# Kernel tuning notes

Measured on AMD Instinct MI355X. Metric: run time of the kernel, lower is better.

The kernel has to match this reference:

```python
import jax, jax.numpy as jnp
import numpy as np

B, N, M = 2, 2048, 1024
C, CTX, H = 1024, 1024, 16
D = C // H
HID = int(C * 4.0)
EPS = 1e-6


def _ln(h):
    # LayerNorm32: fp32 layernorm, eps=1e-6, no affine params
    h32 = h.astype(jnp.float32)
    mu = jnp.mean(h32, axis=-1, keepdims=True)
    var = jnp.var(h32, axis=-1, keepdims=True)
    return ((h32 - mu) * jax.lax.rsqrt(var + EPS)).astype(h.dtype)


def _sdpa(q, k, v):
    # q: [B,Q,H,D], k/v: [B,K,H,D]
    scale = 1.0 / np.sqrt(D)
    s = jnp.einsum('bqhd,bkhd->bhqk', q, k) * scale
    p = jax.nn.softmax(s, axis=-1)
    return jnp.einsum('bhqk,bkhd->bqhd', p, v)


def _forward(x, context, Wqkv, bqkv, Wos, bos, Wq, bq, Wkv, bkv, Woc, boc, W1, b1, W2, b2):
    Bx, Nx, _ = x.shape
    Mx = context.shape[1]
    # --- self-attention (attn_mode='full') ---
    h = _ln(x)
    qkv = (h @ Wqkv + bqkv).reshape(Bx, Nx, 3, H, D)
    q, k, v = qkv[:, :, 0], qkv[:, :, 1], qkv[:, :, 2]
    a = _sdpa(q, k, v).reshape(Bx, Nx, C)
    x = x + (a @ Wos + bos)
    # --- cross-attention (always 'full') ---
    h = _ln(x)
    q = (h @ Wq + bq).reshape(Bx, Nx, H, D)
    kv = (context @ Wkv + bkv).reshape(Bx, Mx, 2, H, D)
    k, v = kv[:, :, 0], kv[:, :, 1]
    a = _sdpa(q, k, v).reshape(Bx, Nx, C)
    x = x + (a @ Woc + boc)
    # --- FFN with tanh-approx GELU ---
    h = _ln(x)
    x = x + (jax.nn.gelu(h @ W1 + b1, approximate=True) @ W2 + b2)
    return x


def setup_inputs() -> dict:
    key = jax.random.key(0)
    ks = jax.random.split(key, 12)
    rn = lambda k, shape: (jax.random.normal(k, shape, jnp.float32) * 0.02)
    return {
        'x': jax.random.normal(ks[0], (B, N, C), jnp.float32),
        'context': jax.random.normal(ks[1], (B, M, CTX), jnp.float32),
        'Wqkv': rn(ks[2], (C, 3 * C)), 'bqkv': jnp.zeros((3 * C,), jnp.float32),
        'Wos': rn(ks[3], (C, C)), 'bos': jnp.zeros((C,), jnp.float32),
        'Wq': rn(ks[4], (C, C)), 'bq': jnp.zeros((C,), jnp.float32),
        'Wkv': rn(ks[5], (CTX, 2 * C)), 'bkv': jnp.zeros((2 * C,), jnp.float32),
        'Woc': rn(ks[6], (C, C)), 'boc': jnp.zeros((C,), jnp.float32),
        'W1': rn(ks[7], (C, HID)), 'b1': jnp.zeros((HID,), jnp.float32),
        'W2': rn(ks[8], (HID, C)), 'b2': jnp.zeros((C,), jnp.float32),
    }


def reference(x, context, Wqkv, bqkv, Wos, bos, Wq, bq, Wkv, bkv, Woc, boc, W1, b1, W2, b2):
    return _forward(x, context, Wqkv, bqkv, Wos, bos, Wq, bq, Wkv, bkv, Woc, boc, W1, b1, W2, b2)
```

## Files before the change

### kernel.cpp

```cpp
#include <hip/hip_runtime.h>
#include <cstdint>

typedef unsigned short u16;
typedef short bf16x8 __attribute__((ext_vector_type(8)));
typedef unsigned short u16x8 __attribute__((ext_vector_type(8)));
typedef float f32x4 __attribute__((ext_vector_type(4)));

__device__ __forceinline__ u16 f2bf(float f) {
  union { float f; uint32_t u; } v; v.f = f;
  uint32_t r = (v.u + 0x7fffu + ((v.u >> 16) & 1u)) >> 16;
  return (u16)r;
}

__device__ __forceinline__ void gload_lds16(const u16* g, u16* l) {
  __builtin_amdgcn_global_load_lds(
      (const __attribute__((address_space(1))) void*)g,
      (__attribute__((address_space(3))) void*)l, 16, 0, 0);
}

__global__ __launch_bounds__(256) void ln_kernel(const float* __restrict__ x,
                                                 u16* __restrict__ h) {
  const int row = blockIdx.x;
  const int tid = threadIdx.x;
  const float4 v = *reinterpret_cast<const float4*>(x + (long)row * 1024 + tid * 4);
  float s  = v.x + v.y + v.z + v.w;
  float ss = v.x * v.x + v.y * v.y + v.z * v.z + v.w * v.w;
#pragma unroll
  for (int off = 32; off >= 1; off >>= 1) {
    s  += __shfl_xor(s, off, 64);
    ss += __shfl_xor(ss, off, 64);
  }
  __shared__ float red[8];
  const int wave = tid >> 6, lane = tid & 63;
  if (lane == 0) { red[wave] = s; red[4 + wave] = ss; }
  __syncthreads();
  s  = red[0] + red[1] + red[2] + red[3];
  ss = red[4] + red[5] + red[6] + red[7];
  const float mu   = s * (1.0f / 1024.0f);
  const float var  = ss * (1.0f / 1024.0f) - mu * mu;
  const float rstd = rsqrtf(var + 1e-6f);
  ushort4 o;
  o.x = f2bf((v.x - mu) * rstd);
  o.y = f2bf((v.y - mu) * rstd);
  o.z = f2bf((v.z - mu) * rstd);
  o.w = f2bf((v.w - mu) * rstd);
  *reinterpret_cast<ushort4*>(h + (long)row * 1024 + tid * 4) = o;
}

struct WEnt { const float* W; u16* Wt; int K, N, tEnd; };
struct WEnts { WEnt e[7]; int n; };

__global__ __launch_bounds__(256) void wconvert_all(WEnts args) {
  __shared__ u16 tile[64][72];
  int t = blockIdx.x;
  int i = 0, tStart = 0;
  while (i < args.n - 1 && t >= args.e[i].tEnd) { tStart = args.e[i].tEnd; i++; }
  const float* W = args.e[i].W;
  u16* Wt = args.e[i].Wt;
  const int K = args.e[i].K, N = args.e[i].N;
  const int rel = t - tStart;
  const int ntn = N >> 6;
  const int tn = rel % ntn, tk = rel / ntn;
  const int n0 = tn * 64, k0 = tk * 64;

  const int th = threadIdx.x;
  const int c4 = (th & 15) * 4;
  const int r  = th >> 4;
#pragma unroll
  for (int ii = 0; ii < 4; ii++) {
    const int row = ii * 16 + r;
    const float4 v = *reinterpret_cast<const float4*>(W + (long)(k0 + row) * N + n0 + c4);
    tile[c4 + 0][row] = f2bf(v.x);
    tile[c4 + 1][row] = f2bf(v.y);
    tile[c4 + 2][row] = f2bf(v.z);
    tile[c4 + 3][row] = f2bf(v.w);
  }
  __syncthreads();
  const int c8 = (th & 7) * 8;
  const int rn = th >> 3;
#pragma unroll
  for (int ii = 0; ii < 2; ii++) {
    const int row = ii * 32 + rn;
    *reinterpret_cast<u16x8*>(Wt + (long)(n0 + row) * K + k0 + c8) =
        *reinterpret_cast<const u16x8*>(&tile[row][c8]);
  }
}

__global__ __launch_bounds__(256) void f2bf_kernel(const float* __restrict__ in,
                                                   u16* __restrict__ out) {
  const long i = ((long)blockIdx.x * 256 + threadIdx.x) * 4;
  const float4 v = *reinterpret_cast<const float4*>(in + i);
  ushort4 o;
  o.x = f2bf(v.x); o.y = f2bf(v.y); o.z = f2bf(v.z); o.w = f2bf(v.w);
  *reinterpret_cast<ushort4*>(out + i) = o;
}

__global__ __launch_bounds__(256) void vtrans(const u16* __restrict__ V,
                                              u16* __restrict__ Vt,
                                              int vStride, long vBatch, int nk) {
  __shared__ u16 tile[64][72];
  const int t = threadIdx.x;
  const int b = blockIdx.z, h = blockIdx.y, n0 = blockIdx.x * 64;
  const u16* vp = V + (long)b * vBatch + h * 64;
  u16* op = Vt + (long)(b * 16 + h) * 64 * (long)nk + n0;
  const int ch = t & 7;
#pragma unroll
  for (int i = 0; i < 2; i++) {
    const int n = (t >> 3) + i * 32;
    const u16x8 v = *reinterpret_cast<const u16x8*>(vp + (long)(n0 + n) * vStride + ch * 8);
#pragma unroll
    for (int j = 0; j < 8; j++) tile[ch * 8 + j][n] = v[j];
  }
  __syncthreads();
#pragma unroll
  for (int i = 0; i < 2; i++) {
    const int d = (t >> 3) + i * 32;
    *reinterpret_cast<u16x8*>(op + (long)d * nk + ch * 8) =
        *reinterpret_cast<const u16x8*>(&tile[d][ch * 8]);
  }
}

template <int TN, int SX, bool OUT_BF16, bool GELU_ACT, bool RES>
__global__ __launch_bounds__(256, 2) void gemm_bt(
    const u16* __restrict__ A, const u16* __restrict__ Bt,
    const float* __restrict__ bias, const float* __restrict__ res,
    void* __restrict__ Cout, int Ndim, int Kdim, int lx, int ly) {
  constexpr int NFRAG = TN / 32;
  __shared__ u16 Al[2][128 * 32];
  __shared__ u16 Bl[2][TN * 32];
  const int j = blockIdx.x;
  const int c = j & 7, kk = j >> 3;
  const int cx = c % SX, cy = c / SX;
  const int bx = cx * lx + (kk % lx);
  const int by = cy * ly + (kk / lx);
  const int m0 = by * 128, n0 = bx * TN;

  const int tid  = threadIdx.x;
  const int lane = tid & 63, wave = tid >> 6;
  const int quad = lane >> 4, l15 = lane & 15;
  const int wr = wave >> 1, wc = wave & 1;

  f32x4 acc[4][NFRAG];
  const f32x4 vzero = {0.f, 0.f, 0.f, 0.f};
#pragma unroll
  for (int i = 0; i < 4; i++)
#pragma unroll
    for (int jj = 0; jj < NFRAG; jj++) acc[i][jj] = vzero;

  const long rowOff = (long)(lane >> 2) * Kdim + (lane & 3) * 8;
  const u16* gA = A  + (long)m0 * Kdim + rowOff;
  const u16* gB = Bt + (long)n0 * Kdim + rowOff;

  auto stage = [&](int k0, int p) {
    gload_lds16(gA + (long)(wave * 16) * Kdim + k0,       &Al[p][wave * 512]);
    gload_lds16(gA + (long)((wave + 4) * 16) * Kdim + k0, &Al[p][(wave + 4) * 512]);
    gload_lds16(gB + (long)(wave * 16) * Kdim + k0,       &Bl[p][wave * 512]);
    if constexpr (TN == 128)
      gload_lds16(gB + (long)((wave + 4) * 16) * Kdim + k0, &Bl[p][(wave + 4) * 512]);
  };

  stage(0, 0);
  int p = 0;
  for (int k0 = 0; k0 < Kdim; k0 += 32, p ^= 1) {
    __syncthreads();
    bf16x8 af[4], bfr[NFRAG];
#pragma unroll
    for (int mt = 0; mt < 4; mt++)
      af[mt] = *reinterpret_cast<const bf16x8*>(&Al[p][(wr * 64 + mt * 16 + l15) * 32 + quad * 8]);
#pragma unroll
    for (int nt = 0; nt < NFRAG; nt++)
      bfr[nt] = *reinterpret_cast<const bf16x8*>(&Bl[p][(wc * NFRAG * 16 + nt * 16 + l15) * 32 + quad * 8]);
    if (k0 + 32 < Kdim) stage(k0 + 32, p ^ 1);
#pragma unroll
    for (int mt = 0; mt < 4; mt++)
#pragma unroll
      for (int nt = 0; nt < NFRAG; nt++)
        acc[mt][nt] = __builtin_amdgcn_mfma_f32_16x16x32_bf16(af[mt], bfr[nt], acc[mt][nt], 0, 0, 0);
  }

#pragma unroll
  for (int nt = 0; nt < NFRAG; nt++) {
    const int col = n0 + wc * NFRAG * 16 + nt * 16 + l15;
    const float bv = bias[col];
#pragma unroll
    for (int mt = 0; mt < 4; mt++) {
#pragma unroll
      for (int r = 0; r < 4; r++) {
        const int row = m0 + wr * 64 + mt * 16 + quad * 4 + r;
        float y = acc[mt][nt][r] + bv;
        if (GELU_ACT) {
          const float t = 0.7978845608028654f * (y + 0.044715f * y * y * y);
          y = 0.5f * y * (1.0f + tanhf(t));
        }
        if (RES) y += res[(long)row * Ndim + col];
        if (OUT_BF16)
          ((u16*)Cout)[(long)row * Ndim + col] = f2bf(y);
        else
          ((float*)Cout)[(long)row * Ndim + col] = y;
      }
    }
  }
}

__global__ __launch_bounds__(256, 2) void attn_kernel(
    const u16* __restrict__ Q, const u16* __restrict__ K, const u16* __restrict__ Vt,
    u16* __restrict__ O, int nk, int qStride, int kStride, int oStride,
    long qBatch, long kBatch, long oBatch) {
  __shared__ u16 Kt[2][64 * 64];
  __shared__ u16 Vl[2][64 * 64];
  __shared__ u16 Pl[4][32 * 64];

  const int tid = threadIdx.x;
  const int lane = tid & 63, wave = tid >> 6;
  const int quad = lane >> 4, l15 = lane & 15;
  const int b = blockIdx.z, hh = blockIdx.y, qt = blockIdx.x;

  const u16* qp = Q + (long)b * qBatch + hh * 64;
  const u16* kp = K + (long)b * kBatch + hh * 64;
  const u16* vp = Vt + (long)(b * 16 + hh) * 64 * (long)nk;

  bf16x8 qf[2][2];
  const int qrow = qt * 128 + wave * 32 + l15;
#pragma unroll
  for (int qg = 0; qg < 2; qg++) {
    qf[qg][0] = *reinterpret_cast<const bf16x8*>(qp + (long)(qrow + qg * 16) * qStride + quad * 8);
    qf[qg][1] = *reinterpret_cast<const bf16x8*>(qp + (long)(qrow + qg * 16) * qStride + 32 + quad * 8);
  }

  const int r8 = lane >> 3;
  const int gcol = ((lane & 7) ^ r8) * 8;
  const u16* kgA = kp + (long)(wave * 8 + r8) * kStride + gcol;
  const u16* kgB = kp + (long)((wave + 4) * 8 + r8) * kStride + gcol;
  const u16* vgA = vp + (long)(wave * 8 + r8) * nk + gcol;
  const u16* vgB = vp + (long)((wave + 4) * 8 + r8) * nk + gcol;

  const int cF = (quad ^ (l15 & 7)) * 8;

  const f32x4 vzero = {0.f, 0.f, 0.f, 0.f};
  f32x4 oAcc[2][4];
  float lSt[2] = {0.f, 0.f};
#pragma unroll
  for (int qg = 0; qg < 2; qg++)
#pragma unroll
    for (int i = 0; i < 4; i++) oAcc[qg][i] = vzero;

  const float SCL = 0.18033688f;
  const int nTiles = nk >> 6;
  const long kAdv = (long)64 * kStride;

  auto stage = [&](int kt, int p) {
    gload_lds16(kgA + kt * kAdv, &Kt[p][wave * 512]);
    gload_lds16(kgB + kt * kAdv, &Kt[p][(wave + 4) * 512]);
    gload_lds16(vgA + kt * 64,   &Vl[p][wave * 512]);
    gload_lds16(vgB + kt * 64,   &Vl[p][(wave + 4) * 512]);
  };

  stage(0, 0);
  int p = 0;
  for (int kt = 0; kt < nTiles; kt++, p ^= 1) {
    __syncthreads();
    if (kt + 1 < nTiles) stage(kt + 1, p ^ 1);

    f32x4 st[2][4];
#pragma unroll
    for (int mt = 0; mt < 4; mt++) {
      const bf16x8 kf0 = *reinterpret_cast<const bf16x8*>(&Kt[p][(mt * 16 + l15) * 64 + cF]);
      const bf16x8 kf1 = *reinterpret_cast<const bf16x8*>(&Kt[p][(mt * 16 + l15) * 64 + (cF ^ 32)]);
#pragma unroll
      for (int qg = 0; qg < 2; qg++) {
        f32x4 z = vzero;
        z = __builtin_amdgcn_mfma_f32_16x16x32_bf16(kf0, qf[qg][0], z, 0, 0, 0);
        z = __builtin_amdgcn_mfma_f32_16x16x32_bf16(kf1, qf[qg][1], z, 0, 0, 0);
        st[qg][mt] = z;
      }
    }

#pragma unroll
    for (int qg = 0; qg < 2; qg++) {
      float ps = 0.f;
#pragma unroll
      for (int mt = 0; mt < 4; mt++)
#pragma unroll
        for (int r = 0; r < 4; r++) {
          const float pw = __builtin_amdgcn_exp2f(st[qg][mt][r] * SCL);
          st[qg][mt][r] = pw;
          ps += pw;
        }
      lSt[qg] += ps;
      u16* plw = &Pl[wave][(qg * 16 + l15) * 64];
#pragma unroll
      for (int mt = 0; mt < 4; mt++) {
        union { float f; uint32_t u; } a0, a1, a2, a3;
        a0.f = st[qg][mt][0]; a1.f = st[qg][mt][1];
        a2.f = st[qg][mt][2]; a3.f = st[qg][mt][3];
        a0.u += 0x8000u; a1.u += 0x8000u; a2.u += 0x8000u; a3.u += 0x8000u;
        uint2 w;
        w.x = __builtin_amdgcn_perm(a1.u, a0.u, 0x07060302u);
        w.y = __builtin_amdgcn_perm(a3.u, a2.u, 0x07060302u);
        const int pcol = (((mt * 2 + (quad >> 1)) ^ (l15 & 7)) * 8) + (quad & 1) * 4;
        *reinterpret_cast<uint2*>(&plw[pcol]) = w;
      }
    }

    bf16x8 pf[2][2];
#pragma unroll
    for (int qg = 0; qg < 2; qg++) {
      const u16* plw = &Pl[wave][(qg * 16 + l15) * 64];
      pf[qg][0] = *reinterpret_cast<const bf16x8*>(&plw[cF]);
      pf[qg][1] = *reinterpret_cast<const bf16x8*>(&plw[cF ^ 32]);
    }
#pragma unroll
    for (int dt = 0; dt < 4; dt++) {
      const bf16x8 vf0 = *reinterpret_cast<const bf16x8*>(&Vl[p][(dt * 16 + l15) * 64 + cF]);
      const bf16x8 vf1 = *reinterpret_cast<const bf16x8*>(&Vl[p][(dt * 16 + l15) * 64 + (cF ^ 32)]);
#pragma unroll
      for (int qg = 0; qg < 2; qg++) {
        oAcc[qg][dt] = __builtin_amdgcn_mfma_f32_16x16x32_bf16(pf[qg][0], vf0, oAcc[qg][dt], 0, 0, 0);
        oAcc[qg][dt] = __builtin_amdgcn_mfma_f32_16x16x32_bf16(pf[qg][1], vf1, oAcc[qg][dt], 0, 0, 0);
      }
    }
  }

  u16* op = O + (long)b * oBatch + hh * 64;
#pragma unroll
  for (int qg = 0; qg < 2; qg++) {
    float l = lSt[qg];
    l += __shfl_xor(l, 16, 64);
    l += __shfl_xor(l, 32, 64);
    float lR[4];
#pragma unroll
    for (int r = 0; r < 4; r++) lR[r] = 1.0f / __shfl(l, quad * 4 + r, 64);
#pragma unroll
    for (int dt = 0; dt < 4; dt++)
#pragma unroll
      for (int r = 0; r < 4; r++) {
        const int row = qt * 128 + wave * 32 + qg * 16 + quad * 4 + r;
        op[(long)row * oStride + dt * 16 + l15] = f2bf(oAcc[qg][dt][r] * lR[r]);
      }
  }
}

extern "C" void kernel_launch(void* const* d_in, const int* in_sizes, int n_in,
                              void* d_out, int out_size, void* d_ws, size_t ws_size,
                              hipStream_t stream) {
  const float* x    = (const float*)d_in[0];
  const float* ctx  = (const float*)d_in[1];
  const float* Wqkv = (const float*)d_in[2];
  const float* bqkv = (const float*)d_in[3];
  const float* Wos  = (const float*)d_in[4];
  const float* bos  = (const float*)d_in[5];
  const float* Wq   = (const float*)d_in[6];
  const float* bq   = (const float*)d_in[7];
  const float* Wkv  = (const float*)d_in[8];
  const float* bkv  = (const float*)d_in[9];
  const float* Woc  = (const float*)d_in[10];
  const float* boc  = (const float*)d_in[11];
  const float* W1   = (const float*)d_in[12];
  const float* b1   = (const float*)d_in[13];
  const float* W2   = (const float*)d_in[14];
  const float* b2   = (const float*)d_in[15];
  float* out = (float*)d_out;
  char* ws = (char*)d_ws;
  const size_t MB = 1024 * 1024;

  if (ws_size >= 80 * MB) {
    u16* Wqkvt = (u16*)(ws + 0 * MB);
    u16* Wost  = (u16*)(ws + 6 * MB);
    u16* Wqt   = (u16*)(ws + 8 * MB);
    u16* Wkvt  = (u16*)(ws + 10 * MB);
    u16* Woct  = (u16*)(ws + 14 * MB);
    u16* W1t   = (u16*)(ws + 16 * MB);
    u16* W2t   = (u16*)(ws + 24 * MB);
    u16* h     = (u16*)(ws + 32 * MB);
    u16* abuf  = (u16*)(ws + 40 * MB);
    u16* qkv   = (u16*)(ws + 48 * MB);
    u16* q2    = (u16*)(ws + 48 * MB);
    u16* kv2   = (u16*)(ws + 56 * MB);
    u16* ctxbf = (u16*)(ws + 64 * MB);
    u16* VtCr  = (u16*)(ws + 68 * MB);
    u16* hid   = (u16*)(ws + 48 * MB);
    u16* VtSelf = h;

    WEnts we;
    we.n = 7;
    we.e[0] = {Wqkv, Wqkvt, 1024, 3072, 768};
    we.e[1] = {Wos,  Wost,  1024, 1024, 1024};
    we.e[2] = {Wq,   Wqt,   1024, 1024, 1280};
    we.e[3] = {Wkv,  Wkvt,  1024, 2048, 1792};
    we.e[4] = {Woc,  Woct,  1024, 1024, 2048};
    we.e[5] = {W1,   W1t,   1024, 4096, 3072};
    we.e[6] = {W2,   W2t,   4096, 1024, 4096};
    wconvert_all<<<dim3(4096), dim3(256), 0, stream>>>(we);
    f2bf_kernel<<<dim3(2048), dim3(256), 0, stream>>>(ctx, ctxbf);

    ln_kernel<<<dim3(4096), dim3(256), 0, stream>>>(x, h);
    gemm_bt<128, 2, true, false, false><<<dim3(768), dim3(256), 0, stream>>>(
        h, Wqkvt, bqkv, nullptr, qkv, 3072, 1024, 12, 8);
    vtrans<<<dim3(32, 16, 2), dim3(256), 0, stream>>>(
        qkv + 2048, VtSelf, 3072, (long)2048 * 3072, 2048);
    attn_kernel<<<dim3(16, 16, 2), dim3(256), 0, stream>>>(
        qkv, qkv + 1024, VtSelf, abuf, 2048, 3072, 3072, 1024,
        (long)2048 * 3072, (long)2048 * 3072, (long)2048 * 1024);
    gemm_bt<64, 1, false, false, true><<<dim3(512), dim3(256), 0, stream>>>(
        abuf, Wost, bos, x, out, 1024, 1024, 16, 4);
    ln_kernel<<<dim3(4096), dim3(256), 0, stream>>>(out, h);
    gemm_bt<64, 1, true, false, false><<<dim3(512), dim3(256), 0, stream>>>(
        h, Wqt, bq, nullptr, q2, 1024, 1024, 16, 4);
    gemm_bt<64, 2, true, false, false><<<dim3(512), dim3(256), 0, stream>>>(
        ctxbf, Wkvt, bkv, nullptr, kv2, 2048, 1024, 16, 4);
    vtrans<<<dim3(16, 16, 2), dim3(256), 0, stream>>>(
        kv2 + 1024, VtCr, 2048, (long)1024 * 2048, 1024);
    attn_kernel<<<dim3(16, 16, 2), dim3(256), 0, stream>>>(
        q2, kv2, VtCr, abuf, 1024, 1024, 2048, 1024,
        (long)2048 * 1024, (long)1024 * 2048, (long)2048 * 1024);
    gemm_bt<64, 1, false, false, true><<<dim3(512), dim3(256), 0, stream>>>(
        abuf, Woct, boc, out, out, 1024, 1024, 16, 4);
    ln_kernel<<<dim3(4096), dim3(256), 0, stream>>>(out, h);
    gemm_bt<128, 2, true, true, false><<<dim3(1024), dim3(256), 0, stream>>>(
        h, W1t, b1, nullptr, hid, 4096, 1024, 16, 8);
    gemm_bt<128, 2, false, false, true><<<dim3(256), dim3(256), 0, stream>>>(
        hid, W2t, b2, out, out, 1024, 4096, 4, 8);
  } else {
    u16* h      = (u16*)ws;
    u16* wbuf   = (u16*)(ws + 8 * MB);
    char* C0    = ws + 16 * MB;
    u16* qkv    = (u16*)C0;
    u16* Wqkvt  = (u16*)(C0 + 24 * MB);
    u16* Wost   = (u16*)C0;
    u16* q2     = (u16*)C0;
    u16* kv2    = (u16*)(C0 + 8 * MB);
    u16* Wqt    = (u16*)(C0 + 16 * MB);
    u16* Wkvt   = (u16*)(C0 + 16 * MB);
    u16* ctxbf  = (u16*)(C0 + 20 * MB);
    u16* VtCr   = (u16*)(C0 + 24 * MB);
    u16* Woct   = (u16*)(C0 + 16 * MB);
    u16* hid    = (u16*)C0;
    u16* VtSelf = h;
    u16* abuf   = wbuf;
    u16* W1t    = wbuf;
    u16* W2t    = wbuf;
    WEnts w1; w1.n = 1;

    ln_kernel<<<dim3(4096), dim3(256), 0, stream>>>(x, h);
    w1.e[0] = {Wqkv, Wqkvt, 1024, 3072, 768};
    wconvert_all<<<dim3(768), dim3(256), 0, stream>>>(w1);
    gemm_bt<128, 2, true, false, false><<<dim3(768), dim3(256), 0, stream>>>(
        h, Wqkvt, bqkv, nullptr, qkv, 3072, 1024, 12, 8);
    vtrans<<<dim3(32, 16, 2), dim3(256), 0, stream>>>(
        qkv + 2048, VtSelf, 3072, (long)2048 * 3072, 2048);
    attn_kernel<<<dim3(16, 16, 2), dim3(256), 0, stream>>>(
        qkv, qkv + 1024, VtSelf, abuf, 2048, 3072, 3072, 1024,
        (long)2048 * 3072, (long)2048 * 3072, (long)2048 * 1024);
    w1.e[0] = {Wos, Wost, 1024, 1024, 256};
    wconvert_all<<<dim3(256), dim3(256), 0, stream>>>(w1);
    gemm_bt<64, 1, false, false, true><<<dim3(512), dim3(256), 0, stream>>>(
        abuf, Wost, bos, x, out, 1024, 1024, 16, 4);
    ln_kernel<<<dim3(4096), dim3(256), 0, stream>>>(out, h);
    w1.e[0] = {Wq, Wqt, 1024, 1024, 256};
    wconvert_all<<<dim3(256), dim3(256), 0, stream>>>(w1);
    gemm_bt<64, 1, true, false, false><<<dim3(512), dim3(256), 0, stream>>>(
        h, Wqt, bq, nullptr, q2, 1024, 1024, 16, 4);
    f2bf_kernel<<<dim3(2048), dim3(256), 0, stream>>>(ctx, ctxbf);
    w1.e[0] = {Wkv, Wkvt, 1024, 2048, 512};
    wconvert_all<<<dim3(512), dim3(256), 0, stream>>>(w1);
    gemm_bt<64, 2, true, false, false><<<dim3(512), dim3(256), 0, stream>>>(
        ctxbf, Wkvt, bkv, nullptr, kv2, 2048, 1024, 16, 4);
    vtrans<<<dim3(16, 16, 2), dim3(256), 0, stream>>>(
        kv2 + 1024, VtCr, 2048, (long)1024 * 2048, 1024);
    attn_kernel<<<dim3(16, 16, 2), dim3(256), 0, stream>>>(
        q2, kv2, VtCr, abuf, 1024, 1024, 2048, 1024,
        (long)2048 * 1024, (long)1024 * 2048, (long)2048 * 1024);
    w1.e[0] = {Woc, Woct, 1024, 1024, 256};
    wconvert_all<<<dim3(256), dim3(256), 0, stream>>>(w1);
    gemm_bt<64, 1, false, false, true><<<dim3(512), dim3(256), 0, stream>>>(
        abuf, Woct, boc, out, out, 1024, 1024, 16, 4);
    ln_kernel<<<dim3(4096), dim3(256), 0, stream>>>(out, h);
    w1.e[0] = {W1, W1t, 1024, 4096, 1024};
    wconvert_all<<<dim3(1024), dim3(256), 0, stream>>>(w1);
    gemm_bt<128, 2, true, true, false><<<dim3(1024), dim3(256), 0, stream>>>(
        h, W1t, b1, nullptr, hid, 4096, 1024, 16, 8);
    w1.e[0] = {W2, W2t, 4096, 1024, 1024};
    wconvert_all<<<dim3(1024), dim3(256), 0, stream>>>(w1);
    gemm_bt<128, 2, false, false, true><<<dim3(256), dim3(256), 0, stream>>>(
        hid, W2t, b2, out, out, 1024, 4096, 4, 8);
  }
}
```

Measured before the change: 486.0 us.

## Split-K the residual output GEMMs with atomic accumulation into output

Adds an ATOMIC split-K mode to the bf16 GEMM. Each blockIdx.y slice covers one part of K and atomically adds its partial sum into the fp32 output, which already holds the residual, and only slice 0 adds the bias. The cross-attention output projection uses 2 K-splits and the FFN down-projection (K=4096, previously only 256 blocks) uses 4. This is meant to fill more compute units on the under-occupied GEMMs, at the cost of atomic traffic and a summation order that varies from run to run.

```diff
diff --git a/kernel.cpp b/kernel.cpp
--- a/kernel.cpp
+++ b/kernel.cpp
@@ -120,11 +120,11 @@
   }
 }
 
-template <int TN, int SX, bool OUT_BF16, bool GELU_ACT, bool RES>
+template <int TN, int SX, bool OUT_BF16, bool GELU_ACT, bool RES, bool ATOMIC>
 __global__ __launch_bounds__(256, 2) void gemm_bt(
     const u16* __restrict__ A, const u16* __restrict__ Bt,
     const float* __restrict__ bias, const float* __restrict__ res,
-    void* __restrict__ Cout, int Ndim, int Kdim, int lx, int ly) {
+    void* __restrict__ Cout, int Ndim, int lx, int ly, int KC, int Kdim) {
   constexpr int NFRAG = TN / 32;
   __shared__ u16 Al[2][128 * 32];
   __shared__ u16 Bl[2][TN * 32];
@@ -134,6 +134,8 @@
   const int bx = cx * lx + (kk % lx);
   const int by = cy * ly + (kk / lx);
   const int m0 = by * 128, n0 = bx * TN;
+  const int kc = ATOMIC ? blockIdx.y : 0;
+  const int kOff = kc * KC;
 
   const int tid  = threadIdx.x;
   const int lane = tid & 63, wave = tid >> 6;
@@ -159,9 +161,10 @@
       gload_lds16(gB + (long)((wave + 4) * 16) * Kdim + k0, &Bl[p][(wave + 4) * 512]);
   };
 
-  stage(0, 0);
+  stage(kOff, 0);
   int p = 0;
-  for (int k0 = 0; k0 < Kdim; k0 += 32, p ^= 1) {
+  const int kEnd = kOff + KC;
+  for (int k0 = kOff; k0 < kEnd; k0 += 32, p ^= 1) {
     __syncthreads();
     bf16x8 af[4], bfr[NFRAG];
 #pragma unroll
@@ -170,7 +173,7 @@
 #pragma unroll
     for (int nt = 0; nt < NFRAG; nt++)
       bfr[nt] = *reinterpret_cast<const bf16x8*>(&Bl[p][(wc * NFRAG * 16 + nt * 16 + l15) * 32 + quad * 8]);
-    if (k0 + 32 < Kdim) stage(k0 + 32, p ^ 1);
+    if (k0 + 32 < kEnd) stage(k0 + 32, p ^ 1);
 #pragma unroll
     for (int mt = 0; mt < 4; mt++)
 #pragma unroll
@@ -187,16 +190,22 @@
 #pragma unroll
       for (int r = 0; r < 4; r++) {
         const int row = m0 + wr * 64 + mt * 16 + quad * 4 + r;
-        float y = acc[mt][nt][r] + bv;
-        if (GELU_ACT) {
-          const float t = 0.7978845608028654f * (y + 0.044715f * y * y * y);
-          y = 0.5f * y * (1.0f + tanhf(t));
+        float y = acc[mt][nt][r];
+        if (ATOMIC) {
+          if (kc == 0) y += bv;
+          atomicAdd((float*)Cout + (long)row * Ndim + col, y);
+        } else {
+          y += bv;
+          if (GELU_ACT) {
+            const float t = 0.7978845608028654f * (y + 0.044715f * y * y * y);
+            y = 0.5f * y * (1.0f + tanhf(t));
+          }
+          if (RES) y += res[(long)row * Ndim + col];
+          if (OUT_BF16)
+            ((u16*)Cout)[(long)row * Ndim + col] = f2bf(y);
+          else
+            ((float*)Cout)[(long)row * Ndim + col] = y;
         }
-        if (RES) y += res[(long)row * Ndim + col];
-        if (OUT_BF16)
-          ((u16*)Cout)[(long)row * Ndim + col] = f2bf(y);
-        else
-          ((float*)Cout)[(long)row * Ndim + col] = y;
       }
     }
   }
@@ -394,32 +403,32 @@
     f2bf_kernel<<<dim3(2048), dim3(256), 0, stream>>>(ctx, ctxbf);
 
     ln_kernel<<<dim3(4096), dim3(256), 0, stream>>>(x, h);
-    gemm_bt<128, 2, true, false, false><<<dim3(768), dim3(256), 0, stream>>>(
-        h, Wqkvt, bqkv, nullptr, qkv, 3072, 1024, 12, 8);
+    gemm_bt<128, 2, true, false, false, false><<<dim3(768), dim3(256), 0, stream>>>(
+        h, Wqkvt, bqkv, nullptr, qkv, 3072, 12, 8, 1024, 1024);
     vtrans<<<dim3(32, 16, 2), dim3(256), 0, stream>>>(
         qkv + 2048, VtSelf, 3072, (long)2048 * 3072, 2048);
     attn_kernel<<<dim3(16, 16, 2), dim3(256), 0, stream>>>(
         qkv, qkv + 1024, VtSelf, abuf, 2048, 3072, 3072, 1024,
         (long)2048 * 3072, (long)2048 * 3072, (long)2048 * 1024);
-    gemm_bt<64, 1, false, false, true><<<dim3(512), dim3(256), 0, stream>>>(
-        abuf, Wost, bos, x, out, 1024, 1024, 16, 4);
+    gemm_bt<64, 1, false, false, true, false><<<dim3(512), dim3(256), 0, stream>>>(
+        abuf, Wost, bos, x, out, 1024, 16, 4, 1024, 1024);
     ln_kernel<<<dim3(4096), dim3(256), 0, stream>>>(out, h);
-    gemm_bt<64, 1, true, false, false><<<dim3(512), dim3(256), 0, stream>>>(
-        h, Wqt, bq, nullptr, q2, 1024, 1024, 16, 4);
-    gemm_bt<64, 2, true, false, false><<<dim3(512), dim3(256), 0, stream>>>(
-        ctxbf, Wkvt, bkv, nullptr, kv2, 2048, 1024, 16, 4);
+    gemm_bt<64, 1, true, false, false, false><<<dim3(512), dim3(256), 0, stream>>>(
+        h, Wqt, bq, nullptr, q2, 1024, 16, 4, 1024, 1024);
+    gemm_bt<64, 2, true, false, false, false><<<dim3(512), dim3(256), 0, stream>>>(
+        ctxbf, Wkvt, bkv, nullptr, kv2, 2048, 16, 4, 1024, 1024);
     vtrans<<<dim3(16, 16, 2), dim3(256), 0, stream>>>(
         kv2 + 1024, VtCr, 2048, (long)1024 * 2048, 1024);
     attn_kernel<<<dim3(16, 16, 2), dim3(256), 0, stream>>>(
         q2, kv2, VtCr, abuf, 1024, 1024, 2048, 1024,
         (long)2048 * 1024, (long)1024 * 2048, (long)2048 * 1024);
-    gemm_bt<64, 1, false, false, true><<<dim3(512), dim3(256), 0, stream>>>(
-        abuf, Woct, boc, out, out, 1024, 1024, 16, 4);
+    gemm_bt<64, 1, false, false, false, true><<<dim3(512, 2), dim3(256), 0, stream>>>(
+        abuf, Woct, boc, nullptr, out, 1024, 16, 4, 512, 1024);
     ln_kernel<<<dim3(4096), dim3(256), 0, stream>>>(out, h);
-    gemm_bt<128, 2, true, true, false><<<dim3(1024), dim3(256), 0, stream>>>(
-        h, W1t, b1, nullptr, hid, 4096, 1024, 16, 8);
-    gemm_bt<128, 2, false, false, true><<<dim3(256), dim3(256), 0, stream>>>(
-        hid, W2t, b2, out, out, 1024, 4096, 4, 8);
+    gemm_bt<128, 2, true, true, false, false><<<dim3(1024), dim3(256), 0, stream>>>(
+        h, W1t, b1, nullptr, hid, 4096, 16, 8, 1024, 1024);
+    gemm_bt<128, 2, false, false, false, true><<<dim3(256, 4), dim3(256), 0, stream>>>(
+        hid, W2t, b2, nullptr, out, 1024, 4, 8, 1024, 4096);
   } else {
     u16* h      = (u16*)ws;
     u16* wbuf   = (u16*)(ws + 8 * MB);
@@ -444,8 +453,8 @@
     ln_kernel<<<dim3(4096), dim3(256), 0, stream>>>(x, h);
     w1.e[0] = {Wqkv, Wqkvt, 1024, 3072, 768};
     wconvert_all<<<dim3(768), dim3(256), 0, stream>>>(w1);
-    gemm_bt<128, 2, true, false, false><<<dim3(768), dim3(256), 0, stream>>>(
-        h, Wqkvt, bqkv, nullptr, qkv, 3072, 1024, 12, 8);
+    gemm_bt<128, 2, true, false, false, false><<<dim3(768), dim3(256), 0, stream>>>(
+        h, Wqkvt, bqkv, nullptr, qkv, 3072, 12, 8, 1024, 1024);
     vtrans<<<dim3(32, 16, 2), dim3(256), 0, stream>>>(
         qkv + 2048, VtSelf, 3072, (long)2048 * 3072, 2048);
     attn_kernel<<<dim3(16, 16, 2), dim3(256), 0, stream>>>(
@@ -453,18 +462,18 @@
         (long)2048 * 3072, (long)2048 * 3072, (long)2048 * 1024);
     w1.e[0] = {Wos, Wost, 1024, 1024, 256};
     wconvert_all<<<dim3(256), dim3(256), 0, stream>>>(w1);
-    gemm_bt<64, 1, false, false, true><<<dim3(512), dim3(256), 0, stream>>>(
-        abuf, Wost, bos, x, out, 1024, 1024, 16, 4);
+    gemm_bt<64, 1, false, false, true, false><<<dim3(512), dim3(256), 0, stream>>>(
+        abuf, Wost, bos, x, out, 1024, 16, 4, 1024, 1024);
     ln_kernel<<<dim3(4096), dim3(256), 0, stream>>>(out, h);
     w1.e[0] = {Wq, Wqt, 1024, 1024, 256};
     wconvert_all<<<dim3(256), dim3(256), 0, stream>>>(w1);
-    gemm_bt<64, 1, true, false, false><<<dim3(512), dim3(256), 0, stream>>>(
-        h, Wqt, bq, nullptr, q2, 1024, 1024, 16, 4);
+    gemm_bt<64, 1, true, false, false, false><<<dim3(512), dim3(256), 0, stream>>>(
+        h, Wqt, bq, nullptr, q2, 1024, 16, 4, 1024, 1024);
     f2bf_kernel<<<dim3(2048), dim3(256), 0, stream>>>(ctx, ctxbf);
     w1.e[0] = {Wkv, Wkvt, 1024, 2048, 512};
     wconvert_all<<<dim3(512), dim3(256), 0, stream>>>(w1);
-    gemm_bt<64, 2, true, false, false><<<dim3(512), dim3(256), 0, stream>>>(
-        ctxbf, Wkvt, bkv, nullptr, kv2, 2048, 1024, 16, 4);
+    gemm_bt<64, 2, true, false, false, false><<<dim3(512), dim3(256), 0, stream>>>(
+        ctxbf, Wkvt, bkv, nullptr, kv2, 2048, 16, 4, 1024, 1024);
     vtrans<<<dim3(16, 16, 2), dim3(256), 0, stream>>>(
         kv2 + 1024, VtCr, 2048, (long)1024 * 2048, 1024);
     attn_kernel<<<dim3(16, 16, 2), dim3(256), 0, stream>>>(
@@ -472,16 +481,16 @@
         (long)2048 * 1024, (long)1024 * 2048, (long)2048 * 1024);
     w1.e[0] = {Woc, Woct, 1024, 1024, 256};
     wconvert_all<<<dim3(256), dim3(256), 0, stream>>>(w1);
-    gemm_bt<64, 1, false, false, true><<<dim3(512), dim3(256), 0, stream>>>(
-        abuf, Woct, boc, out, out, 1024, 1024, 16, 4);
+    gemm_bt<64, 1, false, false, false, true><<<dim3(512, 2), dim3(256), 0, stream>>>(
+        abuf, Woct, boc, nullptr, out, 1024, 16, 4, 512, 1024);
     ln_kernel<<<dim3(4096), dim3(256), 0, stream>>>(out, h);
     w1.e[0] = {W1, W1t, 1024, 4096, 1024};
     wconvert_all<<<dim3(1024), dim3(256), 0, stream>>>(w1);
-    gemm_bt<128, 2, true, true, false><<<dim3(1024), dim3(256), 0, stream>>>(
-        h, W1t, b1, nullptr, hid, 4096, 1024, 16, 8);
+    gemm_bt<128, 2, true, true, false, false><<<dim3(1024), dim3(256), 0, stream>>>(
+        h, W1t, b1, nullptr, hid, 4096, 16, 8, 1024, 1024);
     w1.e[0] = {W2, W2t, 4096, 1024, 1024};
     wconvert_all<<<dim3(1024), dim3(256), 0, stream>>>(w1);
-    gemm_bt<128, 2, false, false, true><<<dim3(256), dim3(256), 0, stream>>>(
-        hid, W2t, b2, out, out, 1024, 4096, 4, 8);
-  }
-}
+    gemm_bt<128, 2, false, false, false, true><<<dim3(256, 4), dim3(256), 0, stream>>>(
+        hid, W2t, b2, nullptr, out, 1024, 4, 8, 1024, 4096);
+  }
+}
```

Result: slower. 516.6 us (+6.3%).
